# Performance work log

Hardware: AMD Instinct MI355X
Metric: run time of the kernel (lower is better)

Reference implementation:

```python
import jax, jax.numpy as jnp
import numpy as np

N = 200000   # num_nodes
D = 64       # embedding_dims
B = 4096     # batch of target nodes (batched per-edge processing)
K = 128      # padded in-neighbor count per target
W = 20       # window_size (history deque length)
H = 128      # hidden_size


def setup_inputs() -> dict:
    key = jax.random.key(0)
    ks = jax.random.split(key, 14)
    return {
        "adj_time": jax.random.uniform(ks[0], (N,), jnp.float32),          # last-seen times in [0,1)
        "gc": jax.random.uniform(ks[1], (N,), jnp.float32),                 # per-node centrality scalar (dict_gc)
        "cur_time": jnp.ones((1,), jnp.float32),                            # current event time (>= all stored times)
        "neigh_mask": jnp.ones((B, K), jnp.float32),                        # 1 = valid neighbor slot
        "hist_feat": jax.random.normal(ks[2], (B, W, 2 * D), jnp.float32),  # feature_dict[...]['feature'] deque
        "hist_time": jax.random.uniform(ks[3], (B, W), jnp.float32),        # feature_dict[...]['time'] deque
        "t2v_w": jax.random.normal(ks[4], (D,), jnp.float32),               # Time2Vec('cos') weights
        "t2v_b": jax.random.normal(ks[5], (D,), jnp.float32),
        "node_w": jax.random.normal(ks[6], (D,), jnp.float32),              # linear_node: Linear(1, D)
        "node_b": jax.random.normal(ks[7], (D,), jnp.float32),
        "att_w": jax.random.normal(ks[8], (2 * D,), jnp.float32),           # Attention: score = cat(a,b) @ w + b
        "att_b": jax.random.normal(ks[9], (1,), jnp.float32),
        "weight": jax.random.normal(ks[10], (H, 4 * D), jnp.float32) * 0.05,
        "targets": jax.random.randint(ks[11], (B,), 0, N),
        "neigh_idx": jax.random.randint(ks[12], (B, K), 0, N),
    }


def reference(adj_time, gc, cur_time, neigh_mask, hist_feat, hist_time,
              t2v_w, t2v_b, node_w, node_b, att_w, att_b, weight,
              targets, neigh_idx):
    t = cur_time[0]

    def node_encoding(idx):
        # Time2Vec('cos'): first channel linear, rest cos(w*dt+b)
        dt = jnp.abs(t - adj_time[idx])[..., None]            # [..., 1]
        phase = t2v_w * dt + t2v_b                            # [..., D]
        tv = jnp.concatenate([phase[..., :1], jnp.cos(phase[..., 1:])], axis=-1)
        feat = jax.nn.relu(tv + gc[idx][..., None] * node_w + node_b)
        # F.normalize (L2 over feature dim)
        return feat / jnp.maximum(jnp.linalg.norm(feat, axis=-1, keepdims=True), 1e-12)

    tgt_feat = node_encoding(targets)       # [B, D]
    ngh_feat = node_encoding(neigh_idx)     # [B, K, D]

    # Decayer(2, 'log'): time_score = 1 / (2 * log(e + dt))
    time_score = 1.0 / (2.0 * jnp.log(jnp.e + (t - adj_time[neigh_idx])))   # [B, K]
    # Attention score between target and each neighbor encoding
    att = (tgt_feat @ att_w[:D])[:, None] \
        + jnp.einsum("bkd,d->bk", ngh_feat, att_w[D:]) + att_b[0]           # [B, K]
    score = jax.nn.leaky_relu(time_score + att, 0.01) * neigh_mask          # [B, K]
    neigh_agg = jnp.einsum("bk,bkd->bd", score, ngh_feat)                   # [B, D]

    combined = jnp.concatenate([tgt_feat, neigh_agg], axis=-1)              # [B, 2D]

    # History aggregation with Decayer(2, 'rev'): w = 1 / (2 * (1 + dt))
    hist_w = 1.0 / (2.0 * (1.0 + (t - hist_time)))                          # [B, W]
    hist_agg = jnp.einsum("bw,bwd->bd", hist_w, hist_feat)                  # [B, 2D]

    feat4 = jnp.concatenate([hist_agg, combined], axis=-1)                  # [B, 4D]
    return jax.nn.relu(feat4 @ weight.T)                                    # [B, H]
```

## Files before the change

kernel.cpp:

```cpp
#include <hip/hip_runtime.h>
#include <math.h>

#define NN 200000
#define DD 64
#define BB 4096
#define KK 128
#define WW 20
#define HH 128
#define TPB 512
#define RPB 4

__device__ __forceinline__ float fast_rcp(float x) { return __builtin_amdgcn_rcpf(x); }
__device__ __forceinline__ float fast_rsq(float x) { return __builtin_amdgcn_rsqf(x); }

__global__ __launch_bounds__(512, 8) void fused(
    const float* __restrict__ adj_time, const float* __restrict__ gc,
    const float* __restrict__ cur_time, const float* __restrict__ neigh_mask,
    const float* __restrict__ hist_feat, const float* __restrict__ hist_time,
    const float* __restrict__ t2v_w, const float* __restrict__ t2v_b,
    const float* __restrict__ node_w, const float* __restrict__ node_b,
    const float* __restrict__ att_w, const float* __restrict__ att_b,
    const float* __restrict__ weight,
    const int* __restrict__ targets, const int* __restrict__ neigh_idx,
    float* __restrict__ out)
{
    const int b0   = blockIdx.x * RPB;
    const int tid  = threadIdx.x;
    const int lane = tid & 63;
    const int wv   = tid >> 6;

    __shared__ float2 dtg[RPB * KK];
    __shared__ float  wk[RPB * KK];
    __shared__ float  hws[RPB][WW];
    __shared__ float  stL[RPB];
    __shared__ float  tile[RPB * 256];
    __shared__ float  aggp[8][64];
    __shared__ float  wl[128 * 33];

    const float t = cur_time[0];

    float ts_k, m_k;
    {
        int   slot = tid;
        int   idx  = neigh_idx[b0 * KK + slot];
        m_k        = neigh_mask[b0 * KK + slot];
        float at   = adj_time[idx];
        float g    = gc[idx];
        dtg[slot]  = make_float2(fabsf(t - at), g);
        ts_k       = fast_rcp(2.0f * __logf(2.71828182845904523536f + (t - at)));
    }
    if (tid < RPB * WW) {
        int r = tid / WW, w = tid - r * WW;
        hws[r][w] = fast_rcp(2.0f * (1.0f + (t - hist_time[(b0 + r) * WW + w])));
    }
    if (wv < RPB) {
        int   tg  = targets[b0 + wv];
        float dtT = fabsf(t - adj_time[tg]);
        float gT  = gc[tg];
        float ph  = fmaf(t2v_w[lane], dtT, t2v_b[lane]);
        float tv_ = (lane == 0) ? ph : __cosf(ph);
        float f   = fmaxf(tv_ + fmaf(gT, node_w[lane], node_b[lane]), 0.f);
        float ss  = f * f;
#pragma unroll
        for (int off = 32; off; off >>= 1) ss += __shfl_xor(ss, off, 64);
        float invn = fast_rsq(fmaxf(ss, 1e-24f));
        float tfn  = f * invn;
        float sdt  = tfn * att_w[lane];
#pragma unroll
        for (int off = 32; off; off >>= 1) sdt += __shfl_xor(sdt, off, 64);
        if (lane == 0) stL[wv] = sdt;
        tile[wv * 256 + 128 + lane] = tfn;
    }
    __syncthreads();

    {
        const float ab = att_b[0];
        int    slot = tid;
        int    r    = slot >> 7;
        float2 dg   = dtg[slot];
        float  s2 = 0.f, sd = 0.f;
#pragma unroll 8
        for (int d = 0; d < 64; ++d) {
            float ph  = fmaf(t2v_w[d], dg.x, t2v_b[d]);
            float cv  = __cosf(ph);
            float tv_ = (d == 0) ? ph : cv;
            float f   = fmaxf(tv_ + fmaf(dg.y, node_w[d], node_b[d]), 0.f);
            s2 = fmaf(f, f, s2);
            sd = fmaf(f, att_w[64 + d], sd);
        }
        float invn = fast_rsq(fmaxf(s2, 1e-24f));
        float sc   = ts_k + stL[r] + sd * invn + ab;
        sc = (sc > 0.f) ? sc : 0.01f * sc;
        wk[slot] = sc * m_k * invn;
    }

    {
        int r = tid >> 7, d = tid & 127;
        const float* hf = hist_feat + (size_t)(b0 + r) * WW * 128 + d;
        float s = 0.f;
#pragma unroll
        for (int w = 0; w < WW; ++w) s = fmaf(hws[r][w], hf[w * 128], s);
        tile[r * 256 + d] = s;
    }
    __syncthreads();

    {
        const int r   = wv >> 1;
        const int sub = wv & 1;
        float pw = t2v_w[lane], pb = t2v_b[lane];
        float nw = node_w[lane], nb2 = node_b[lane];
        float acc = 0.f;
        const int base = r * KK + sub * 64;
#pragma unroll 8
        for (int k = 0; k < 64; ++k) {
            float2 dg = dtg[base + k];
            float  w_ = wk[base + k];
            float  ph = fmaf(pw, dg.x, pb);
            float  cv = __cosf(ph);
            float  tv_ = (lane == 0) ? ph : cv;
            float  f  = fmaxf(tv_ + fmaf(dg.y, nw, nb2), 0.f);
            acc = fmaf(w_, f, acc);
        }
        aggp[wv][lane] = acc;
    }
    __syncthreads();

    if ((wv & 1) == 0) {
        int r = wv >> 1;
        tile[r * 256 + 192 + lane] = aggp[wv][lane] + aggp[wv + 1][lane];
    }

    const int h = tid & 127;
    const int r = tid >> 7;
    const float* tb = tile + r * 256;
    float acc = 0.f;

    for (int c = 0; c < 8; ++c) {
        __syncthreads();
#pragma unroll
        for (int i = 0; i < 8; ++i) {
            int l  = i * TPB + tid;
            int hh = l >> 5, jj = l & 31;
            wl[hh * 33 + jj] = weight[hh * 256 + c * 32 + jj];
        }
        __syncthreads();

#pragma unroll
        for (int jj = 0; jj < 32; jj += 4) {
            float w0 = wl[h * 33 + jj + 0];
            float w1 = wl[h * 33 + jj + 1];
            float w2 = wl[h * 33 + jj + 2];
            float w3 = wl[h * 33 + jj + 3];
            float4 f4 = *(const float4*)(tb + c * 32 + jj);
            acc += w0 * f4.x + w1 * f4.y + w2 * f4.z + w3 * f4.w;
        }
    }

    out[(size_t)(b0 + r) * 128 + h] = fmaxf(acc, 0.f);
}

extern "C" void kernel_launch(void* const* d_in, const int* in_sizes, int n_in,
                              void* d_out, int out_size, void* d_ws, size_t ws_size,
                              hipStream_t stream) {
    const float* adj_time  = (const float*)d_in[0];
    const float* gc        = (const float*)d_in[1];
    const float* cur_time  = (const float*)d_in[2];
    const float* neigh_mask= (const float*)d_in[3];
    const float* hist_feat = (const float*)d_in[4];
    const float* hist_time = (const float*)d_in[5];
    const float* t2v_w     = (const float*)d_in[6];
    const float* t2v_b     = (const float*)d_in[7];
    const float* node_w    = (const float*)d_in[8];
    const float* node_b    = (const float*)d_in[9];
    const float* att_w     = (const float*)d_in[10];
    const float* att_b     = (const float*)d_in[11];
    const float* weight    = (const float*)d_in[12];
    const int*   targets   = (const int*)d_in[13];
    const int*   neigh_idx = (const int*)d_in[14];

    float* out = (float*)d_out;

    fused<<<BB / RPB, TPB, 0, stream>>>(adj_time, gc, cur_time, neigh_mask,
                                        hist_feat, hist_time, t2v_w, t2v_b,
                                        node_w, node_b, att_w, att_b, weight,
                                        targets, neigh_idx, out);
}
```

Baseline: 138.6 us.

## Broadcast per-neighbor values via readlane instead of shared memory staging

Per-neighbor dt, gc and the attention weight now stay in registers. The aggregation loop broadcasts them across the wavefront with readlane, which removes the dtg and wk shared arrays and one barrier. The weight tile is loaded with float4 into a 36-padded LDS layout, and the feature tile is read once into registers and broadcast with readlane in the final matvec. This cuts LDS traffic and instruction count, but adds many scalar readlane operations and fully unrolls the 64-iteration loop, which raises code size and register pressure.

```diff
diff --git a/kernel.cpp b/kernel.cpp
--- a/kernel.cpp
+++ b/kernel.cpp
@@ -12,6 +12,9 @@
 
 __device__ __forceinline__ float fast_rcp(float x) { return __builtin_amdgcn_rcpf(x); }
 __device__ __forceinline__ float fast_rsq(float x) { return __builtin_amdgcn_rsqf(x); }
+__device__ __forceinline__ float readlane_f(float v, int l) {
+    return __builtin_bit_cast(float, __builtin_amdgcn_readlane(__builtin_bit_cast(int, v), l));
+}
 
 __global__ __launch_bounds__(512, 8) void fused(
     const float* __restrict__ adj_time, const float* __restrict__ gc,
@@ -28,26 +31,25 @@
     const int tid  = threadIdx.x;
     const int lane = tid & 63;
     const int wv   = tid >> 6;
+    const int r_   = tid >> 7;
+    const int d_   = tid & 127;
 
-    __shared__ float2 dtg[RPB * KK];
-    __shared__ float  wk[RPB * KK];
-    __shared__ float  hws[RPB][WW];
-    __shared__ float  stL[RPB];
-    __shared__ float  tile[RPB * 256];
-    __shared__ float  aggp[8][64];
-    __shared__ float  wl[128 * 33];
+    __shared__ float hws[RPB][WW];
+    __shared__ float stL[RPB];
+    __shared__ float tile[RPB * 256];
+    __shared__ float aggp[8][64];
+    __shared__ float wl[128 * 36];
 
     const float t = cur_time[0];
 
-    float ts_k, m_k;
+    float m_k, at, g, dt, ts_k;
     {
-        int   slot = tid;
-        int   idx  = neigh_idx[b0 * KK + slot];
-        m_k        = neigh_mask[b0 * KK + slot];
-        float at   = adj_time[idx];
-        float g    = gc[idx];
-        dtg[slot]  = make_float2(fabsf(t - at), g);
-        ts_k       = fast_rcp(2.0f * __logf(2.71828182845904523536f + (t - at)));
+        int idx = neigh_idx[b0 * KK + tid];
+        m_k     = neigh_mask[b0 * KK + tid];
+        at      = adj_time[idx];
+        g       = gc[idx];
+        dt      = fabsf(t - at);
+        ts_k    = fast_rcp(2.0f * __logf(2.71828182845904523536f + (t - at)));
     }
     if (tid < RPB * WW) {
         int r = tid / WW, w = tid - r * WW;
@@ -73,90 +75,84 @@
     }
     __syncthreads();
 
+    float wk;
     {
-        const float ab = att_b[0];
-        int    slot = tid;
-        int    r    = slot >> 7;
-        float2 dg   = dtg[slot];
-        float  s2 = 0.f, sd = 0.f;
+        float s2 = 0.f, sd = 0.f;
 #pragma unroll 8
         for (int d = 0; d < 64; ++d) {
-            float ph  = fmaf(t2v_w[d], dg.x, t2v_b[d]);
+            float ph  = fmaf(t2v_w[d], dt, t2v_b[d]);
             float cv  = __cosf(ph);
             float tv_ = (d == 0) ? ph : cv;
-            float f   = fmaxf(tv_ + fmaf(dg.y, node_w[d], node_b[d]), 0.f);
+            float f   = fmaxf(tv_ + fmaf(g, node_w[d], node_b[d]), 0.f);
             s2 = fmaf(f, f, s2);
             sd = fmaf(f, att_w[64 + d], sd);
         }
         float invn = fast_rsq(fmaxf(s2, 1e-24f));
-        float sc   = ts_k + stL[r] + sd * invn + ab;
+        float sc   = ts_k + stL[r_] + sd * invn + att_b[0];
         sc = (sc > 0.f) ? sc : 0.01f * sc;
-        wk[slot] = sc * m_k * invn;
+        wk = sc * m_k * invn;
     }
 
     {
-        int r = tid >> 7, d = tid & 127;
-        const float* hf = hist_feat + (size_t)(b0 + r) * WW * 128 + d;
+        const float* hf = hist_feat + (size_t)(b0 + r_) * WW * 128 + d_;
         float s = 0.f;
 #pragma unroll
-        for (int w = 0; w < WW; ++w) s = fmaf(hws[r][w], hf[w * 128], s);
-        tile[r * 256 + d] = s;
+        for (int w = 0; w < WW; ++w) s = fmaf(hws[r_][w], hf[w * 128], s);
+        tile[r_ * 256 + d_] = s;
     }
-    __syncthreads();
 
     {
-        const int r   = wv >> 1;
-        const int sub = wv & 1;
         float pw = t2v_w[lane], pb = t2v_b[lane];
         float nw = node_w[lane], nb2 = node_b[lane];
         float acc = 0.f;
-        const int base = r * KK + sub * 64;
-#pragma unroll 8
-        for (int k = 0; k < 64; ++k) {
-            float2 dg = dtg[base + k];
-            float  w_ = wk[base + k];
-            float  ph = fmaf(pw, dg.x, pb);
-            float  cv = __cosf(ph);
-            float  tv_ = (lane == 0) ? ph : cv;
-            float  f  = fmaxf(tv_ + fmaf(dg.y, nw, nb2), 0.f);
-            acc = fmaf(w_, f, acc);
+#pragma unroll
+        for (int j = 0; j < 64; ++j) {
+            float dtj = readlane_f(dt, j);
+            float gj  = readlane_f(g,  j);
+            float wkj = readlane_f(wk, j);
+            float ph  = fmaf(pw, dtj, pb);
+            float cv  = __cosf(ph);
+            float tv_ = (lane == 0) ? ph : cv;
+            float f   = fmaxf(tv_ + fmaf(gj, nw, nb2), 0.f);
+            acc = fmaf(wkj, f, acc);
         }
         aggp[wv][lane] = acc;
     }
     __syncthreads();
 
-    if ((wv & 1) == 0) {
-        int r = wv >> 1;
-        tile[r * 256 + 192 + lane] = aggp[wv][lane] + aggp[wv + 1][lane];
-    }
+    if (!(wv & 1))
+        tile[(wv >> 1) * 256 + 192 + lane] = aggp[wv][lane] + aggp[wv | 1][lane];
+    __syncthreads();
 
     const int h = tid & 127;
-    const int r = tid >> 7;
-    const float* tb = tile + r * 256;
+    float4 t4 = *(const float4*)(tile + r_ * 256 + 4 * lane);
     float acc = 0.f;
 
     for (int c = 0; c < 8; ++c) {
         __syncthreads();
 #pragma unroll
-        for (int i = 0; i < 8; ++i) {
+        for (int i = 0; i < 2; ++i) {
             int l  = i * TPB + tid;
-            int hh = l >> 5, jj = l & 31;
-            wl[hh * 33 + jj] = weight[hh * 256 + c * 32 + jj];
+            int hh = l >> 3;
+            int q8 = (l & 7) * 4;
+            float4 w4 = *(const float4*)(weight + hh * 256 + c * 32 + q8);
+            *(float4*)(wl + hh * 36 + q8) = w4;
         }
         __syncthreads();
 
 #pragma unroll
-        for (int jj = 0; jj < 32; jj += 4) {
-            float w0 = wl[h * 33 + jj + 0];
-            float w1 = wl[h * 33 + jj + 1];
-            float w2 = wl[h * 33 + jj + 2];
-            float w3 = wl[h * 33 + jj + 3];
-            float4 f4 = *(const float4*)(tb + c * 32 + jj);
-            acc += w0 * f4.x + w1 * f4.y + w2 * f4.z + w3 * f4.w;
+        for (int q = 0; q < 8; ++q) {
+            float4 w4 = *(const float4*)(wl + h * 36 + 4 * q);
+            int src = c * 8 + q;
+            float tx = readlane_f(t4.x, src);
+            float ty = readlane_f(t4.y, src);
+            float tz = readlane_f(t4.z, src);
+            float tw = readlane_f(t4.w, src);
+            acc += w4.x * tx + w4.y * ty + w4.z * tz + w4.w * tw;
         }
     }
 
-    out[(size_t)(b0 + r) * 128 + h] = fmaxf(acc, 0.f);
+    out[(size_t)(b0 + r_) * 128 + h] = fmaxf(acc, 0.f);
 }
 
 extern "C" void kernel_launch(void* const* d_in, const int* in_sizes, int n_in,
```

Result: no change. 137.9 us (-0.5%).
